# Kernel optimization log

Measured on AMD Instinct MI355X. Metric: run time of the kernel, lower is better.

The kernel has to match this reference:

```python
import jax, jax.numpy as jnp
import numpy as np

B = 16        # graphs per protein batch
NPG = 2000    # nodes per graph
N = B * NPG   # total nodes
E = 640000    # total edges
H, C = 3, 128 # heads, hidden_dim
FIN = 1038
K = 400       # ceil(0.2 * NPG) SAGPool keep count
NEG = 0.1     # LeakyReLU slope in model
EPS = 1e-5


def setup_inputs() -> dict:
    key = jax.random.key(0)
    ks = jax.random.split(key, 24)
    d = {}
    d['p1_x'] = jax.random.normal(ks[0], (N, FIN), jnp.float32)
    d['p2_x'] = jax.random.normal(ks[1], (N, FIN), jnp.float32)
    d['p1_edge_index'] = jax.random.randint(ks[2], (2, E), 0, N, jnp.int32)
    d['p2_edge_index'] = jax.random.randint(ks[3], (2, E), 0, N, jnp.int32)
    d['p1_edge_attr'] = jax.random.uniform(ks[4], (E, 2), jnp.float32)
    d['p2_edge_attr'] = jax.random.uniform(ks[5], (E, 2), jnp.float32)
    s_in = 1.0 / np.sqrt(FIN)
    s_h = 1.0 / np.sqrt(C)
    # GATv2Conv params (lin_l has bias, lin_r no bias, lin_edge, att, out bias)
    d['Wl'] = jax.random.normal(ks[6], (FIN, H * C), jnp.float32) * s_in
    d['bl'] = jnp.zeros((H * C,), jnp.float32)
    d['Wr'] = jax.random.normal(ks[7], (FIN, H * C), jnp.float32) * s_in
    d['We'] = jax.random.normal(ks[8], (2, H * C), jnp.float32) * 0.5
    d['att'] = jax.random.normal(ks[9], (H, C), jnp.float32) * s_h
    d['conv_bias'] = jnp.zeros((C,), jnp.float32)
    # BatchNorm1d
    d['gamma'] = jnp.ones((C,), jnp.float32)
    d['beta'] = jnp.zeros((C,), jnp.float32)
    # SAGPooling scorer: GraphConv(C -> 1)
    d['gc_Wrel'] = jax.random.normal(ks[10], (C, 1), jnp.float32) * s_h
    d['gc_Wroot'] = jax.random.normal(ks[11], (C, 1), jnp.float32) * s_h
    d['gc_b'] = jnp.zeros((1,), jnp.float32)
    # MLP head
    d['W1'] = jax.random.normal(ks[12], (2 * C, C), jnp.float32) / np.sqrt(2 * C)
    d['b1'] = jnp.zeros((C,), jnp.float32)
    d['W2'] = jax.random.normal(ks[13], (C, C // 2), jnp.float32) * s_h
    d['b2'] = jnp.zeros((C // 2,), jnp.float32)
    d['Wo'] = jax.random.normal(ks[14], (C // 2, 1), jnp.float32) / np.sqrt(C // 2)
    d['bo'] = jnp.zeros((1,), jnp.float32)
    return d


def gatv2(x, ei, ea, Wl, bl, Wr, We, att, conv_bias):
    # GATv2Conv, heads=3, concat=False, edge_dim=2, add_self_loops (fill='mean')
    loop = jnp.arange(N, dtype=ei.dtype)
    src = jnp.concatenate([ei[0], loop])
    dst = jnp.concatenate([ei[1], loop])
    ea_full = jnp.concatenate([ea, jnp.broadcast_to(ea.mean(0), (N, ea.shape[1]))], 0)
    xl = (x @ Wl + bl).reshape(N, H, C)
    xr = (x @ Wr).reshape(N, H, C)
    ef = (ea_full @ We).reshape(-1, H, C)
    m = xl[src] + xr[dst] + ef                      # [E+N, H, C]
    e = jnp.einsum('ehc,hc->eh', jax.nn.leaky_relu(m, 0.2), att)
    emax = jax.ops.segment_max(e, dst, num_segments=N)
    ex = jnp.exp(e - emax[dst])
    denom = jax.ops.segment_sum(ex, dst, num_segments=N)
    alpha = ex / denom[dst]                          # softmax per dst node, per head
    out = jax.ops.segment_sum(alpha[:, :, None] * xl[src], dst, num_segments=N)
    return out.mean(1) + conv_bias                   # concat=False -> head mean


def branch(x, ei, ea, Wl, bl, Wr, We, att, conv_bias, gamma, beta,
           gc_Wrel, gc_Wroot, gc_b):
    h = gatv2(x, ei, ea, Wl, bl, Wr, We, att, conv_bias)
    h = jax.nn.leaky_relu(h, NEG)
    mu = h.mean(0)
    var = ((h - mu) ** 2).mean(0)
    h = (h - mu) / jnp.sqrt(var + EPS) * gamma + beta  # BatchNorm1d (batch stats)
    # SAGPooling scorer: GraphConv out_i = W_root x_i + W_rel sum_{j->i} x_j + b
    agg = jax.ops.segment_sum(h[ei[0]], ei[1], num_segments=N)
    score = jnp.tanh((h @ gc_Wroot + agg @ gc_Wrel + gc_b)[:, 0])  # [N]
    s = score.reshape(B, NPG)
    topv, topi = jax.lax.top_k(s, K)                 # per-graph top-k
    hb = h.reshape(B, NPG, C)
    hsel = jnp.take_along_axis(hb, topi[:, :, None], axis=1)  # [B, K, C]
    hsel = hsel * topv[:, :, None]                   # x[perm] * tanh(score)[perm]
    return hsel.mean(1)                              # global mean pool -> [B, C]


def reference(p1_x, p2_x, p1_edge_attr, p2_edge_attr, Wl, bl, Wr, We, att,
              conv_bias, gamma, beta, gc_Wrel, gc_Wroot, gc_b, W1, b1, W2, b2,
              Wo, bo, p1_edge_index, p2_edge_index):
    x1 = branch(p1_x, p1_edge_index, p1_edge_attr, Wl, bl, Wr, We, att,
                conv_bias, gamma, beta, gc_Wrel, gc_Wroot, gc_b)
    x2 = branch(p2_x, p2_edge_index, p2_edge_attr, Wl, bl, Wr, We, att,
                conv_bias, gamma, beta, gc_Wrel, gc_Wroot, gc_b)
    xc = jnp.concatenate([x1, x2], 1)                # [B, 2C]
    xc = jax.nn.leaky_relu(xc @ W1 + b1, NEG)
    xc = jax.nn.leaky_relu(xc @ W2 + b2, NEG)
    return jax.nn.sigmoid(xc @ Wo + bo)              # [B, 1]
```

## Files before the change

### kernel.cpp

```cpp
#include <hip/hip_runtime.h>
#include <hip/hip_bf16.h>
#include <math.h>

#define NN 32000
#define EE 640000
#define CC 128
#define HC 384
#define FIN 1038
#define KP 1056
#define KT 33
#define BB 16
#define NPG 2000
#define KK 400

#define XLR_STR 12288000u
#define HBN_STR 4096000u
#define OFF_STR 32064u

#define XL_OFF     0u
#define XR_OFF     24576000u
#define HBN_OFF    49152000u
#define SSRC_OFF   57344000u
#define SEA_OFF    58624000u
#define CNT_OFF    61184000u
#define BNSUM_OFF  61248000u
#define BNSQ_OFF   61248256u
#define MEANEA_OFF 61248512u
#define ZERO_BYTES ((61248516u - 61184000u) * 4u)
#define OFFS_OFF   61248576u
#define CUR_OFF    61312704u
#define R_OFF      61376704u
#define REL_OFF    61440704u
#define SCORE_OFF  61504704u
#define XB_OFF     61568704u
#define WTH_OFF    61572800u
#define WTL_OFF    61978304u

typedef __attribute__((ext_vector_type(8))) _Float16 f16x8;
typedef __attribute__((ext_vector_type(4))) float f32x4;
typedef __attribute__((ext_vector_type(8))) unsigned short us8;

typedef const __attribute__((address_space(1))) unsigned int* gp1_t;
typedef __attribute__((address_space(3))) unsigned int* lp3_t;
__device__ __forceinline__ void gl_lds16(const void* g, void* l) {
    __builtin_amdgcn_global_load_lds((gp1_t)g, (lp3_t)l, 16, 0, 0);
}

__global__ __launch_bounds__(256) void k_prep(const int* __restrict__ ei0, const int* __restrict__ ei1,
                                              const float* __restrict__ ea0, const float* __restrict__ ea1,
                                              int* __restrict__ cnt, float* __restrict__ meanea) {
    int b = blockIdx.x;
    int br = (b >= 2500);
    int tid = threadIdx.x;
    int e = (b - br * 2500) * 256 + tid;
    const int* ei = br ? ei1 : ei0;
    const float* ea = br ? ea1 : ea0;
    cnt += br * NN; meanea += br * 2;
    float s0 = 0.f, s1 = 0.f;
    if (e < EE) {
        atomicAdd(&cnt[ei[EE + e]], 1);
        float2 t = ((const float2*)ea)[e];
        s0 = t.x; s1 = t.y;
    }
    __shared__ float r0[256], r1[256];
    r0[tid] = s0; r1[tid] = s1; __syncthreads();
    for (int st = 128; st; st >>= 1) {
        if (tid < st) { r0[tid] += r0[tid + st]; r1[tid] += r1[tid + st]; }
        __syncthreads();
    }
    if (tid == 0) { atomicAdd(&meanea[0], r0[0]); atomicAdd(&meanea[1], r1[0]); }
}

__global__ __launch_bounds__(1024) void k_scan(const int* __restrict__ cnt, int* __restrict__ offs, int* __restrict__ cur) {
    int br = blockIdx.x;
    cnt += br * NN; offs += br * OFF_STR; cur += br * NN;
    __shared__ int sb[1024];
    int tid = threadIdx.x;
    int base = tid * 32;
    int s = 0;
    for (int i = 0; i < 32; i++) { int idx = base + i; s += (idx < NN) ? cnt[idx] : 0; }
    sb[tid] = s; __syncthreads();
    for (int off = 1; off < 1024; off <<= 1) {
        int v = (tid >= off) ? sb[tid - off] : 0;
        __syncthreads();
        sb[tid] += v;
        __syncthreads();
    }
    int run = sb[tid] - s;
    for (int i = 0; i < 32; i++) {
        int idx = base + i;
        if (idx < NN) { int c = cnt[idx]; offs[idx] = run; cur[idx] = run; run += c; }
    }
    if (tid == 1023) offs[NN] = run;
}

__global__ __launch_bounds__(256) void k_scatter(const int* __restrict__ ei0, const int* __restrict__ ei1,
                                                 const float* __restrict__ ea0, const float* __restrict__ ea1,
                                                 int* __restrict__ cur, int* __restrict__ ssrc, float2* __restrict__ sea) {
    int b = blockIdx.x;
    int br = (b >= 2500);
    int e = (b - br * 2500) * 256 + threadIdx.x;
    const int* ei = br ? ei1 : ei0;
    const float* ea = br ? ea1 : ea0;
    cur += br * NN; ssrc += br * EE; sea += br * EE;
    if (e < EE) {
        int d = ei[EE + e];
        int p = atomicAdd(&cur[d], 1);
        ssrc[p] = ei[e];
        sea[p] = ((const float2*)ea)[e];
    }
}

__global__ __launch_bounds__(256) void k_cvtW(const float* __restrict__ Wl_, const float* __restrict__ Wr_,
                                              unsigned short* __restrict__ Bh) {
    int idx = blockIdx.x * 256 + threadIdx.x;
    if (idx >= 768 * (KP / 8)) return;
    int n = idx / (KP / 8);
    int seg = idx - n * (KP / 8);
    int c0 = seg * 8;
    const float* W = (n < HC) ? Wl_ : Wr_;
    int nc = (n < HC) ? n : n - HC;
    us8 h8;
#pragma unroll
    for (int j = 0; j < 8; ++j) {
        int k = c0 + j;
        float v = (k < FIN) ? W[(size_t)k * HC + nc] : 0.f;
        _Float16 h = (_Float16)v;
        h8[j] = __builtin_bit_cast(unsigned short, h);
    }
    *(us8*)&Bh[(size_t)n * KP + c0] = h8;
}

__global__ __launch_bounds__(256) void k_gemm2f(const float* __restrict__ x0, const float* __restrict__ x1,
                                                const unsigned short* __restrict__ Bh,
                                                const float* __restrict__ bias, float* __restrict__ ws) {
    __shared__ _Float16 sA[128 * 32], sB[128 * 32];
    const int bid = blockIdx.x;
    const int br = (bid >= 1504);
    const int b2 = br ? (bid - 1504) : bid;
    const float* x = br ? x1 : x0;
    float* xl = ws + XL_OFF + br * XLR_STR;
    float* xr = ws + XR_OFF + br * XLR_STR;

    const int xcd = b2 & 7, slot = b2 >> 3;
    const int t = xcd * 188 + slot;
    if (t >= 1500) return;
    const int mt = t / 6, nt = t - mt * 6;
    const int bm = mt * 128, bn = nt * 128;

    const int tid = threadIdx.x;
    const int wave = tid >> 6, lane = tid & 63;
    const int wm = (wave >> 1) * 64, wn = (wave & 1) * 64;
    const int quad = lane >> 4, l15 = lane & 15;

    const int srow = wave * 16 + (lane >> 2);
    const int scol = (lane & 3) * 8;
    const size_t gB0 = (size_t)(bn + srow) * KP + scol;
    const size_t gB1 = (size_t)(bn + 64 + srow) * KP + scol;
    const int lB0 = (wave * 16) * 32 + lane * 8;
    const int lB1 = (64 + wave * 16) * 32 + lane * 8;

    const int arow0 = wave * 32 + (lane >> 2);
    const int acol = (lane & 3) * 8;

    f32x4 acc[4][4];
#pragma unroll
    for (int i = 0; i < 4; ++i)
#pragma unroll
        for (int j = 0; j < 4; ++j) {
            f32x4 z = {0.f, 0.f, 0.f, 0.f};
            acc[i][j] = z;
        }

    const int aoff0 = (wm + l15) * 32 + quad * 8;
    const int boff0 = (wn + l15) * 32 + quad * 8;

    for (int kt = 0; kt < KT; ++kt) {
        const int kc = kt * 32;
        gl_lds16(Bh + gB0 + kc, &sB[lB0]);
        gl_lds16(Bh + gB1 + kc, &sB[lB1]);
        int gcol = kc + acol;
        if (gcol >= FIN) gcol = 0;
#pragma unroll
        for (int rep = 0; rep < 2; ++rep) {
            const int lrow = arow0 + rep * 16;
            const float* gp = x + (size_t)(bm + lrow) * FIN + gcol;
            float2 v01 = ((const float2*)gp)[0];
            float2 v23 = ((const float2*)gp)[1];
            float2 v45 = ((const float2*)gp)[2];
            float2 v67 = ((const float2*)gp)[3];
            f16x8 a;
            a[0] = (_Float16)v01.x; a[1] = (_Float16)v01.y;
            a[2] = (_Float16)v23.x; a[3] = (_Float16)v23.y;
            a[4] = (_Float16)v45.x; a[5] = (_Float16)v45.y;
            a[6] = (_Float16)v67.x; a[7] = (_Float16)v67.y;
            const int lidx = lrow * 32 + acol;
            *(f16x8*)&sA[lidx] = a;
        }
        __syncthreads();
        f16x8 b[4];
#pragma unroll
        for (int j = 0; j < 4; ++j) b[j] = *(const f16x8*)&sB[boff0 + j * 512];
#pragma unroll
        for (int i = 0; i < 4; ++i) {
            f16x8 a = *(const f16x8*)&sA[aoff0 + i * 512];
#pragma unroll
            for (int j = 0; j < 4; ++j)
                acc[i][j] = __builtin_amdgcn_mfma_f32_16x16x32_f16(a, b[j], acc[i][j], 0, 0, 0);
        }
        __syncthreads();
    }

    const bool isL = (nt < 3);
    float* outp = isL ? xl : xr;
    const int nbase = isL ? bn : (bn - HC);
#pragma unroll
    for (int j = 0; j < 4; ++j) {
        const int ncol = wn + j * 16 + l15;
        const float bj = isL ? bias[bn + ncol] : 0.f;
#pragma unroll
        for (int i = 0; i < 4; ++i) {
#pragma unroll
            for (int r = 0; r < 4; ++r) {
                int m = bm + wm + i * 16 + quad * 4 + r;
                outp[(size_t)m * HC + nbase + ncol] = acc[i][j][r] + bj;
            }
        }
    }
}

__global__ __launch_bounds__(256) void k_gat(const float* __restrict__ xlb, const float* __restrict__ xrb,
                                             const int* __restrict__ offsb, const int* __restrict__ ssrcb,
                                             const float2* __restrict__ seab, const float* __restrict__ meaneab,
                                             const float* __restrict__ We, const float* __restrict__ att,
                                             const float* __restrict__ conv_bias, float* __restrict__ houtb) {
    int gwave = (blockIdx.x * 256 + threadIdx.x) >> 6;
    int lane = threadIdx.x & 63;
    int br = (gwave >= NN);
    int wave = gwave - br * NN;
    const float* xl = xlb + br * XLR_STR;
    const float* xr = xrb + br * XLR_STR;
    const int* offs = offsb + br * OFF_STR;
    const int* ssrc = ssrcb + br * EE;
    const float2* sea = seab + br * EE;
    const float* meanea = meaneab + br * 2;
    float* hout = houtb + br * HBN_STR;

    float we0[6], we1[6], attv[6], xrv[6];
#pragma unroll
    for (int j = 0; j < 6; j++) {
        int i = j * 64 + lane;
        we0[j] = We[i]; we1[j] = We[HC + i]; attv[j] = att[i];
        xrv[j] = xr[(size_t)wave * HC + i];
    }
    float me0 = meanea[0] * (1.0f / EE), me1 = meanea[1] * (1.0f / EE);
    float acc[6] = {0, 0, 0, 0, 0, 0};
    float den0 = 0, den1 = 0, den2 = 0;
    int p0 = offs[wave], p1 = offs[wave + 1];
    for (int p = p0 - 1; p < p1; ++p) {
        int s; float ea0, ea1;
        if (p < p0) { s = wave; ea0 = me0; ea1 = me1; }
        else { s = ssrc[p]; float2 t = sea[p]; ea0 = t.x; ea1 = t.y; }
        const float* xls = xl + (size_t)s * HC;
        float xv[6], pr0 = 0, pr1 = 0, pr2 = 0;
#pragma unroll
        for (int j = 0; j < 6; j++) {
            float v = xls[j * 64 + lane];
            xv[j] = v;
            float m = v + xrv[j] + ea0 * we0[j] + ea1 * we1[j];
            float t = (m > 0.f) ? m : 0.2f * m;
            float c = t * attv[j];
            if (j < 2) pr0 += c; else if (j < 4) pr1 += c; else pr2 += c;
        }
#pragma unroll
        for (int mask = 32; mask; mask >>= 1) {
            pr0 += __shfl_xor(pr0, mask);
            pr1 += __shfl_xor(pr1, mask);
            pr2 += __shfl_xor(pr2, mask);
        }
        float w0 = __expf(pr0), w1 = __expf(pr1), w2 = __expf(pr2);
        den0 += w0; den1 += w1; den2 += w2;
        acc[0] += w0 * xv[0]; acc[1] += w0 * xv[1];
        acc[2] += w1 * xv[2]; acc[3] += w1 * xv[3];
        acc[4] += w2 * xv[4]; acc[5] += w2 * xv[5];
    }
    float i0 = 1.f / den0, i1 = 1.f / den1, i2 = 1.f / den2;
    float o0 = (acc[0] * i0 + acc[2] * i1 + acc[4] * i2) * (1.f / 3.f) + conv_bias[lane];
    float o1 = (acc[1] * i0 + acc[3] * i1 + acc[5] * i2) * (1.f / 3.f) + conv_bias[64 + lane];
    o0 = (o0 > 0.f) ? o0 : 0.1f * o0;
    o1 = (o1 > 0.f) ? o1 : 0.1f * o1;
    hout[(size_t)wave * CC + lane] = o0;
    hout[(size_t)wave * CC + 64 + lane] = o1;
}

__global__ __launch_bounds__(256) void k_bnstats(const float* __restrict__ hb, float* __restrict__ bnsumb, float* __restrict__ bnsqb) {
    int b = blockIdx.x;
    int br = b >> 9, lb = b & 511;
    const float* h = hb + br * HBN_STR;
    float* bnsum = bnsumb + br * CC;
    float* bnsq = bnsqb + br * CC;
    int c = threadIdx.x & 127;
    int row0 = lb * 2 + (threadIdx.x >> 7);
    float s = 0.f, ss = 0.f;
    for (int n = row0; n < NN; n += 1024) {
        float v = h[(size_t)n * CC + c];
        s += v; ss += v * v;
    }
    atomicAdd(&bnsum[c], s);
    atomicAdd(&bnsq[c], ss);
}

__global__ __launch_bounds__(256) void k_bnapply(float* __restrict__ hb, const float* __restrict__ bnsumb,
                                                 const float* __restrict__ bnsqb,
                                                 const float* __restrict__ gamma, const float* __restrict__ beta,
                                                 const float* __restrict__ wroot,
                                                 const float* __restrict__ wrel, float* __restrict__ r_b, float* __restrict__ rel_b) {
    int gwave = (blockIdx.x * 256 + threadIdx.x) >> 6;
    int lane = threadIdx.x & 63;
    int br = (gwave >= NN);
    int wave = gwave - br * NN;
    float* h = hb + br * HBN_STR;
    const float* bnsum = bnsumb + br * CC;
    const float* bnsq = bnsqb + br * CC;
    float* r_ = r_b + br * NN;
    float* rel_ = rel_b + br * NN;

    float mu0 = bnsum[lane] * (1.f / NN);
    float var0 = bnsq[lane] * (1.f / NN) - mu0 * mu0;
    float sc0 = gamma[lane] * rsqrtf(var0 + 1e-5f);
    float sh0 = beta[lane] - mu0 * sc0;
    float mu1 = bnsum[64 + lane] * (1.f / NN);
    float var1 = bnsq[64 + lane] * (1.f / NN) - mu1 * mu1;
    float sc1 = gamma[64 + lane] * rsqrtf(var1 + 1e-5f);
    float sh1 = beta[64 + lane] - mu1 * sc1;

    size_t base = (size_t)wave * CC;
    float v0 = h[base + lane], v1 = h[base + 64 + lane];
    v0 = v0 * sc0 + sh0;
    v1 = v1 * sc1 + sh1;
    h[base + lane] = v0;
    h[base + 64 + lane] = v1;
    float pr = v0 * wroot[lane] + v1 * wroot[64 + lane];
    float pl = v0 * wrel[lane] + v1 * wrel[64 + lane];
#pragma unroll
    for (int m = 32; m; m >>= 1) {
        pr += __shfl_xor(pr, m);
        pl += __shfl_xor(pl, m);
    }
    if (lane == 0) { r_[wave] = pr; rel_[wave] = pl; }
}

__global__ __launch_bounds__(256) void k_score(const float* __restrict__ r_b, const float* __restrict__ rel_b,
                                               const int* __restrict__ offsb, const int* __restrict__ ssrcb,
                                               const float* __restrict__ gcb, float* __restrict__ scoreb) {
    int gwave = (blockIdx.x * 256 + threadIdx.x) >> 6;
    int lane = threadIdx.x & 63;
    int br = (gwave >= NN);
    int wave = gwave - br * NN;
    const float* r_ = r_b + br * NN;
    const float* rel_ = rel_b + br * NN;
    const int* offs = offsb + br * OFF_STR;
    const int* ssrc = ssrcb + br * EE;
    float* score = scoreb + br * NN;
    int p0 = offs[wave], p1 = offs[wave + 1];
    float s = 0.f;
    for (int p = p0 + lane; p < p1; p += 64) s += rel_[ssrc[p]];
#pragma unroll
    for (int m = 32; m; m >>= 1) s += __shfl_xor(s, m);
    if (lane == 0) score[wave] = tanhf(r_[wave] + s + gcb[0]);
}

__global__ __launch_bounds__(1024) void k_topk(const float* __restrict__ scoreb, const float* __restrict__ hb,
                                               float* __restrict__ xbout) {
    __shared__ float sv[2048];
    __shared__ int si[2048];
    __shared__ float red[8][128];
    int b = blockIdx.x, tid = threadIdx.x;
    int br = b >> 4, g = b & 15;
    const float* score = scoreb + br * NN;
    const float* h = hb + br * HBN_STR;
    for (int i = tid; i < 2048; i += 1024) {
        sv[i] = (i < NPG) ? score[g * NPG + i] : -2.0f;
        si[i] = i;
    }
    __syncthreads();
    for (int k = 2; k <= 2048; k <<= 1) {
        for (int j = k >> 1; j > 0; j >>= 1) {
            for (int t = tid; t < 2048; t += 1024) {
                int ixj = t ^ j;
                if (ixj > t) {
                    bool up = ((t & k) == 0);
                    float a = sv[t], bv = sv[ixj];
                    bool sw = up ? (a < bv) : (a > bv);
                    if (sw) {
                        sv[t] = bv; sv[ixj] = a;
                        int tmp = si[t]; si[t] = si[ixj]; si[ixj] = tmp;
                    }
                }
            }
            __syncthreads();
        }
    }
    int grp = tid >> 7, c = tid & 127;
    float a = 0.f;
    for (int kk = grp; kk < KK; kk += 8) {
        int node = g * NPG + si[kk];
        a += sv[kk] * h[(size_t)node * CC + c];
    }
    red[grp][c] = a;
    __syncthreads();
    if (tid < 128) {
        float v = (red[0][tid] + red[1][tid] + red[2][tid] + red[3][tid] +
                   red[4][tid] + red[5][tid] + red[6][tid] + red[7][tid]) * (1.f / KK);
        xbout[(br * BB + g) * CC + tid] = v;
    }
}

__global__ __launch_bounds__(128) void k_mlp(const float* __restrict__ xb, const float* __restrict__ W1,
                                             const float* __restrict__ b1, const float* __restrict__ W2,
                                             const float* __restrict__ b2, const float* __restrict__ Wo,
                                             const float* __restrict__ bo, float* __restrict__ out) {
    int g = blockIdx.x, tid = threadIdx.x;
    __shared__ float xc[256], l1[128], l2[64];
    xc[tid] = xb[g * CC + tid];
    xc[128 + tid] = xb[BB * CC + g * CC + tid];
    __syncthreads();
    float s = b1[tid];
    for (int i = 0; i < 256; i++) s += xc[i] * W1[i * 128 + tid];
    l1[tid] = (s > 0.f) ? s : 0.1f * s;
    __syncthreads();
    if (tid < 64) {
        float s2 = b2[tid];
        for (int i = 0; i < 128; i++) s2 += l1[i] * W2[i * 64 + tid];
        l2[tid] = (s2 > 0.f) ? s2 : 0.1f * s2;
    }
    __syncthreads();
    if (tid < 64) {
        float p = l2[tid] * Wo[tid];
#pragma unroll
        for (int m = 32; m; m >>= 1) p += __shfl_xor(p, m);
        if (tid == 0) out[g] = 1.f / (1.f + __expf(-(p + bo[0])));
    }
}

extern "C" void kernel_launch(void* const* d_in, const int* in_sizes, int n_in,
                              void* d_out, int out_size, void* d_ws, size_t ws_size,
                              hipStream_t stream) {
    (void)in_sizes; (void)n_in; (void)out_size; (void)ws_size;
    const float* x0   = (const float*)d_in[0];
    const float* x1   = (const float*)d_in[1];
    const int*   ei0  = (const int*)d_in[2];
    const int*   ei1  = (const int*)d_in[3];
    const float* ea0  = (const float*)d_in[4];
    const float* ea1  = (const float*)d_in[5];
    const float* Wl   = (const float*)d_in[6];
    const float* bl   = (const float*)d_in[7];
    const float* Wr   = (const float*)d_in[8];
    const float* We   = (const float*)d_in[9];
    const float* att  = (const float*)d_in[10];
    const float* cb   = (const float*)d_in[11];
    const float* gam  = (const float*)d_in[12];
    const float* bet  = (const float*)d_in[13];
    const float* wrel = (const float*)d_in[14];
    const float* wroot= (const float*)d_in[15];
    const float* gcb  = (const float*)d_in[16];
    const float* W1   = (const float*)d_in[17];
    const float* b1   = (const float*)d_in[18];
    const float* W2   = (const float*)d_in[19];
    const float* b2   = (const float*)d_in[20];
    const float* Wo   = (const float*)d_in[21];
    const float* bo   = (const float*)d_in[22];

    float* ws = (float*)d_ws;
    float*  xl    = ws + XL_OFF;
    float*  xr    = ws + XR_OFF;
    float*  hbn   = ws + HBN_OFF;
    int*    ssrc  = (int*)(ws + SSRC_OFF);
    float2* sea   = (float2*)(ws + SEA_OFF);
    int*    cnt   = (int*)(ws + CNT_OFF);
    float*  bnsum = ws + BNSUM_OFF;
    float*  bnsq  = ws + BNSQ_OFF;
    float*  meanea= ws + MEANEA_OFF;
    int*    offs  = (int*)(ws + OFFS_OFF);
    int*    cur   = (int*)(ws + CUR_OFF);
    float*  r_    = ws + R_OFF;
    float*  rel_  = ws + REL_OFF;
    float*  score = ws + SCORE_OFF;
    float*  xb    = ws + XB_OFF;
    unsigned short* Wth = (unsigned short*)(ws + WTH_OFF);

    hipMemsetAsync(cnt, 0, ZERO_BYTES, stream);
    k_cvtW<<<(768 * (KP / 8) + 255) / 256, 256, 0, stream>>>(Wl, Wr, Wth);

    k_prep<<<5000, 256, 0, stream>>>(ei0, ei1, ea0, ea1, cnt, meanea);
    k_scan<<<2, 1024, 0, stream>>>(cnt, offs, cur);
    k_scatter<<<5000, 256, 0, stream>>>(ei0, ei1, ea0, ea1, cur, ssrc, sea);

    k_gemm2f<<<3008, 256, 0, stream>>>(x0, x1, Wth, bl, ws);

    k_gat<<<16000, 256, 0, stream>>>(xl, xr, offs, ssrc, sea, meanea, We, att, cb, hbn);

    k_bnstats<<<1024, 256, 0, stream>>>(hbn, bnsum, bnsq);
    k_bnapply<<<16000, 256, 0, stream>>>(hbn, bnsum, bnsq, gam, bet, wroot, wrel, r_, rel_);
    k_score<<<16000, 256, 0, stream>>>(r_, rel_, offs, ssrc, gcb, score);
    k_topk<<<32, 1024, 0, stream>>>(score, hbn, xb);

    k_mlp<<<BB, 128, 0, stream>>>(xb, W1, b1, W2, b2, Wo, bo, (float*)d_out);
}
```

Baseline: 1.298 ms.

## Store xl in fp16 and process two edges per wave in GAT aggregation

New measurement: 1.244 ms. 1.04x faster.

```diff
diff --git a/kernel.cpp b/kernel.cpp
--- a/kernel.cpp
+++ b/kernel.cpp
@@ -34,9 +34,9 @@
 #define SCORE_OFF  61504704u
 #define XB_OFF     61568704u
 #define WTH_OFF    61572800u
-#define WTL_OFF    61978304u
 
 typedef __attribute__((ext_vector_type(8))) _Float16 f16x8;
+typedef __attribute__((ext_vector_type(2))) _Float16 f16x2;
 typedef __attribute__((ext_vector_type(4))) float f32x4;
 typedef __attribute__((ext_vector_type(8))) unsigned short us8;
 
@@ -139,7 +139,7 @@
     const int br = (bid >= 1504);
     const int b2 = br ? (bid - 1504) : bid;
     const float* x = br ? x1 : x0;
-    float* xl = ws + XL_OFF + br * XLR_STR;
+    _Float16* xlh = (_Float16*)(ws + XL_OFF) + (size_t)br * XLR_STR;
     float* xr = ws + XR_OFF + br * XLR_STR;
 
     const int xcd = b2 & 7, slot = b2 >> 3;
@@ -212,33 +212,48 @@
     }
 
     const bool isL = (nt < 3);
-    float* outp = isL ? xl : xr;
-    const int nbase = isL ? bn : (bn - HC);
-#pragma unroll
-    for (int j = 0; j < 4; ++j) {
-        const int ncol = wn + j * 16 + l15;
-        const float bj = isL ? bias[bn + ncol] : 0.f;
-#pragma unroll
-        for (int i = 0; i < 4; ++i) {
-#pragma unroll
-            for (int r = 0; r < 4; ++r) {
-                int m = bm + wm + i * 16 + quad * 4 + r;
-                outp[(size_t)m * HC + nbase + ncol] = acc[i][j][r] + bj;
+    if (isL) {
+#pragma unroll
+        for (int j = 0; j < 4; ++j) {
+            const int ncol = wn + j * 16 + l15;
+            const float bj = bias[bn + ncol];
+#pragma unroll
+            for (int i = 0; i < 4; ++i) {
+#pragma unroll
+                for (int r = 0; r < 4; ++r) {
+                    int m = bm + wm + i * 16 + quad * 4 + r;
+                    xlh[(size_t)m * HC + bn + ncol] = (_Float16)(acc[i][j][r] + bj);
+                }
             }
         }
-    }
-}
-
-__global__ __launch_bounds__(256) void k_gat(const float* __restrict__ xlb, const float* __restrict__ xrb,
+    } else {
+        const int nbase = bn - HC;
+#pragma unroll
+        for (int j = 0; j < 4; ++j) {
+            const int ncol = wn + j * 16 + l15;
+#pragma unroll
+            for (int i = 0; i < 4; ++i) {
+#pragma unroll
+                for (int r = 0; r < 4; ++r) {
+                    int m = bm + wm + i * 16 + quad * 4 + r;
+                    xr[(size_t)m * HC + nbase + ncol] = acc[i][j][r];
+                }
+            }
+        }
+    }
+}
+
+__global__ __launch_bounds__(256) void k_gat(const unsigned short* __restrict__ xlhb, const float* __restrict__ xrb,
                                              const int* __restrict__ offsb, const int* __restrict__ ssrcb,
                                              const float2* __restrict__ seab, const float* __restrict__ meaneab,
                                              const float* __restrict__ We, const float* __restrict__ att,
                                              const float* __restrict__ conv_bias, float* __restrict__ houtb) {
     int gwave = (blockIdx.x * 256 + threadIdx.x) >> 6;
     int lane = threadIdx.x & 63;
+    int half = lane >> 5, l32 = lane & 31;
     int br = (gwave >= NN);
-    int wave = gwave - br * NN;
-    const float* xl = xlb + br * XLR_STR;
+    int node = gwave - br * NN;
+    const _Float16* xlh = (const _Float16*)xlhb + (size_t)br * XLR_STR;
     const float* xr = xrb + br * XLR_STR;
     const int* offs = offsb + br * OFF_STR;
     const int* ssrc = ssrcb + br * EE;
@@ -246,51 +261,111 @@
     const float* meanea = meaneab + br * 2;
     float* hout = houtb + br * HBN_STR;
 
-    float we0[6], we1[6], attv[6], xrv[6];
-#pragma unroll
-    for (int j = 0; j < 6; j++) {
-        int i = j * 64 + lane;
-        we0[j] = We[i]; we1[j] = We[HC + i]; attv[j] = att[i];
-        xrv[j] = xr[(size_t)wave * HC + i];
+    f16x2 we0p[6], we1p[6], attp[6], xrp[6];
+    const float2* xrw = (const float2*)(xr + (size_t)node * HC);
+#pragma unroll
+    for (int jj = 0; jj < 6; ++jj) {
+        int q = l32 + 32 * jj;
+        float2 w0 = ((const float2*)We)[q];
+        float2 w1 = ((const float2*)(We + HC))[q];
+        float2 av = ((const float2*)att)[q];
+        float2 xv = xrw[q];
+        we0p[jj][0] = (_Float16)w0.x; we0p[jj][1] = (_Float16)w0.y;
+        we1p[jj][0] = (_Float16)w1.x; we1p[jj][1] = (_Float16)w1.y;
+        attp[jj][0] = (_Float16)av.x; attp[jj][1] = (_Float16)av.y;
+        xrp[jj][0]  = (_Float16)xv.x; xrp[jj][1]  = (_Float16)xv.y;
     }
     float me0 = meanea[0] * (1.0f / EE), me1 = meanea[1] * (1.0f / EE);
-    float acc[6] = {0, 0, 0, 0, 0, 0};
-    float den0 = 0, den1 = 0, den2 = 0;
-    int p0 = offs[wave], p1 = offs[wave + 1];
-    for (int p = p0 - 1; p < p1; ++p) {
-        int s; float ea0, ea1;
-        if (p < p0) { s = wave; ea0 = me0; ea1 = me1; }
-        else { s = ssrc[p]; float2 t = sea[p]; ea0 = t.x; ea1 = t.y; }
-        const float* xls = xl + (size_t)s * HC;
-        float xv[6], pr0 = 0, pr1 = 0, pr2 = 0;
-#pragma unroll
-        for (int j = 0; j < 6; j++) {
-            float v = xls[j * 64 + lane];
-            xv[j] = v;
-            float m = v + xrv[j] + ea0 * we0[j] + ea1 * we1[j];
-            float t = (m > 0.f) ? m : 0.2f * m;
-            float c = t * attv[j];
-            if (j < 2) pr0 += c; else if (j < 4) pr1 += c; else pr2 += c;
-        }
-#pragma unroll
-        for (int mask = 32; mask; mask >>= 1) {
-            pr0 += __shfl_xor(pr0, mask);
-            pr1 += __shfl_xor(pr1, mask);
-            pr2 += __shfl_xor(pr2, mask);
-        }
-        float w0 = __expf(pr0), w1 = __expf(pr1), w2 = __expf(pr2);
+
+    int p0 = offs[node], p1 = offs[node + 1];
+    int cntE = p1 - p0;
+    int iters = (cntE + 2) >> 1;
+
+    float den0 = 0.f, den1 = 0.f, den2 = 0.f;
+    float accv[12];
+#pragma unroll
+    for (int k = 0; k < 12; ++k) accv[k] = 0.f;
+
+    const f16x2 zero2 = {(_Float16)0.f, (_Float16)0.f};
+    const f16x2 c02 = {(_Float16)0.2f, (_Float16)0.2f};
+
+    for (int i = 0; i < iters; ++i) {
+        int t = 2 * i + half;
+        bool self = (t == 0);
+        bool valid = (t <= cntE);
+        int p = p0 + t - 1;
+        if (p < p0) p = p0;
+        if (p > EE - 1) p = EE - 1;
+        int sv = ssrc[p];
+        float2 ev = sea[p];
+        int s = self ? node : sv;
+        float ea0 = self ? me0 : ev.x;
+        float ea1 = self ? me1 : ev.y;
+        f16x2 e0p, e1p;
+        e0p[0] = (_Float16)ea0; e0p[1] = e0p[0];
+        e1p[0] = (_Float16)ea1; e1p[1] = e1p[0];
+
+        const f16x2* xrow = (const f16x2*)(xlh + (size_t)s * HC);
+        f16x2 xv[6];
+#pragma unroll
+        for (int jj = 0; jj < 6; ++jj) xv[jj] = xrow[l32 + 32 * jj];
+
+        float pr0 = 0.f, pr1 = 0.f, pr2 = 0.f;
+#pragma unroll
+        for (int jj = 0; jj < 6; ++jj) {
+            f16x2 u = xrp[jj] + e0p * we0p[jj];
+            u = u + e1p * we1p[jj];
+            f16x2 m = xv[jj] + u;
+            f16x2 mx = __builtin_elementwise_max(m, zero2);
+            f16x2 mn = __builtin_elementwise_min(m, zero2);
+            f16x2 lk = mx + mn * c02;
+#if __has_builtin(__builtin_amdgcn_fdot2)
+            if (jj < 2)      pr0 = __builtin_amdgcn_fdot2(lk, attp[jj], pr0, false);
+            else if (jj < 4) pr1 = __builtin_amdgcn_fdot2(lk, attp[jj], pr1, false);
+            else             pr2 = __builtin_amdgcn_fdot2(lk, attp[jj], pr2, false);
+#else
+            float c = (float)lk[0] * (float)attp[jj][0] + (float)lk[1] * (float)attp[jj][1];
+            if (jj < 2) pr0 += c; else if (jj < 4) pr1 += c; else pr2 += c;
+#endif
+        }
+#pragma unroll
+        for (int msk = 16; msk; msk >>= 1) {
+            pr0 += __shfl_xor(pr0, msk);
+            pr1 += __shfl_xor(pr1, msk);
+            pr2 += __shfl_xor(pr2, msk);
+        }
+        float w0 = valid ? __expf(pr0) : 0.f;
+        float w1 = valid ? __expf(pr1) : 0.f;
+        float w2 = valid ? __expf(pr2) : 0.f;
         den0 += w0; den1 += w1; den2 += w2;
-        acc[0] += w0 * xv[0]; acc[1] += w0 * xv[1];
-        acc[2] += w1 * xv[2]; acc[3] += w1 * xv[3];
-        acc[4] += w2 * xv[4]; acc[5] += w2 * xv[5];
-    }
-    float i0 = 1.f / den0, i1 = 1.f / den1, i2 = 1.f / den2;
-    float o0 = (acc[0] * i0 + acc[2] * i1 + acc[4] * i2) * (1.f / 3.f) + conv_bias[lane];
-    float o1 = (acc[1] * i0 + acc[3] * i1 + acc[5] * i2) * (1.f / 3.f) + conv_bias[64 + lane];
-    o0 = (o0 > 0.f) ? o0 : 0.1f * o0;
-    o1 = (o1 > 0.f) ? o1 : 0.1f * o1;
-    hout[(size_t)wave * CC + lane] = o0;
-    hout[(size_t)wave * CC + 64 + lane] = o1;
+#pragma unroll
+        for (int jj = 0; jj < 6; ++jj) {
+            float wh = (jj < 2) ? w0 : ((jj < 4) ? w1 : w2);
+            accv[2 * jj]     += wh * (float)xv[jj][0];
+            accv[2 * jj + 1] += wh * (float)xv[jj][1];
+        }
+    }
+
+#pragma unroll
+    for (int k = 0; k < 12; ++k) accv[k] += __shfl_xor(accv[k], 32);
+    den0 += __shfl_xor(den0, 32);
+    den1 += __shfl_xor(den1, 32);
+    den2 += __shfl_xor(den2, 32);
+
+    if (half == 0) {
+        float i0 = 1.f / den0, i1 = 1.f / den1, i2 = 1.f / den2;
+#pragma unroll
+        for (int jja = 0; jja < 2; ++jja) {
+#pragma unroll
+            for (int b = 0; b < 2; ++b) {
+                int c = (((jja * 32 + l32) << 1) | b);
+                float o = (accv[2 * jja + b] * i0 + accv[2 * (jja + 2) + b] * i1 +
+                           accv[2 * (jja + 4) + b] * i2) * (1.f / 3.f) + conv_bias[c];
+                o = (o > 0.f) ? o : 0.1f * o;
+                hout[(size_t)node * CC + c] = o;
+            }
+        }
+    }
 }
 
 __global__ __launch_bounds__(256) void k_bnstats(const float* __restrict__ hb, float* __restrict__ bnsumb, float* __restrict__ bnsqb) {
@@ -472,8 +547,6 @@
     const float* bo   = (const float*)d_in[22];
 
     float* ws = (float*)d_ws;
-    float*  xl    = ws + XL_OFF;
-    float*  xr    = ws + XR_OFF;
     float*  hbn   = ws + HBN_OFF;
     int*    ssrc  = (int*)(ws + SSRC_OFF);
     float2* sea   = (float2*)(ws + SEA_OFF);
@@ -488,6 +561,8 @@
     float*  score = ws + SCORE_OFF;
     float*  xb    = ws + XB_OFF;
     unsigned short* Wth = (unsigned short*)(ws + WTH_OFF);
+    unsigned short* xlh = (unsigned short*)(ws + XL_OFF);
+    float*  xr    = ws + XR_OFF;
 
     hipMemsetAsync(cnt, 0, ZERO_BYTES, stream);
     k_cvtW<<<(768 * (KP / 8) + 255) / 256, 256, 0, stream>>>(Wl, Wr, Wth);
@@ -498,7 +573,7 @@
 
     k_gemm2f<<<3008, 256, 0, stream>>>(x0, x1, Wth, bl, ws);
 
-    k_gat<<<16000, 256, 0, stream>>>(xl, xr, offs, ssrc, sea, meanea, We, att, cb, hbn);
+    k_gat<<<16000, 256, 0, stream>>>(xlh, xr, offs, ssrc, sea, meanea, We, att, cb, hbn);
 
     k_bnstats<<<1024, 256, 0, stream>>>(hbn, bnsum, bnsq);
     k_bnapply<<<16000, 256, 0, stream>>>(hbn, bnsum, bnsq, gam, bet, wroot, wrel, r_, rel_);
```
